# Kernel optimization log

Measured on AMD Instinct MI355X. Metric: run time of the kernel, lower is better.

## Reference

```python
import jax, jax.numpy as jnp
import numpy as np

B, T, C, H = 256, 256, 384, 64
MAX_REL = 3  # max_relative_position hardcoded in module


def setup_inputs() -> dict:
    key = jax.random.key(0)
    ks = jax.random.split(key, 6)
    s = 1.0 / np.sqrt(C)
    return {
        "x": jax.random.normal(ks[0], (B, T, C), dtype=jnp.float32),
        "Wq": jax.random.normal(ks[1], (C, H), dtype=jnp.float32) * s,
        "Wk": jax.random.normal(ks[2], (C, H), dtype=jnp.float32) * s,
        "Wv": jax.random.normal(ks[3], (C, H), dtype=jnp.float32) * s,
        "rel_k_table": jax.random.normal(ks[4], (2 * MAX_REL + 1, H), dtype=jnp.float32) * s,
        "rel_v_table": jax.random.normal(ks[5], (2 * MAX_REL + 1, H), dtype=jnp.float32) * s,
    }


def reference(x, Wq, Wk, Wv, rel_k_table, rel_v_table):
    Bd, Td, Cd = x.shape
    Hd = Wq.shape[1]
    q = x @ Wq  # [B,T,H]
    k = x @ Wk
    v = x @ Wv
    # relative position indices, clipped Shaw-style
    r = jnp.arange(Td)
    idx = jnp.clip(r[None, :] - r[:, None], -MAX_REL, MAX_REL) + MAX_REL  # [T,T]
    rk = rel_k_table[idx]  # [T,T,H]
    rv = rel_v_table[idx]  # [T,T,H]
    attn1 = jnp.einsum('bth,bsh->bts', q, k)
    attn2 = jnp.einsum('bth,tsh->bts', q, rk)
    scale = jnp.sqrt(jnp.asarray(Hd, dtype=x.dtype))
    scores = (attn1 + attn2) / scale
    causal = jnp.tril(jnp.ones((Td, Td), dtype=bool))
    scores = jnp.where(causal[None, :, :], scores, -jnp.inf)
    attn = jax.nn.softmax(scores, axis=-1)  # dropout = identity (eval mode)
    w1 = jnp.einsum('bts,bsh->bth', attn, v)
    w2 = jnp.einsum('bts,tsh->bth', attn, rv)
    return w1 + w2  # [B,T,H]
```

## Files before the change

### kernel.cpp

```cpp
#include <hip/hip_runtime.h>
#include <hip/hip_bf16.h>


typedef __attribute__((ext_vector_type(8))) __bf16 bf16x8;
typedef __attribute__((ext_vector_type(8))) short short8;
typedef __attribute__((ext_vector_type(4))) float f32x4;
typedef __attribute__((ext_vector_type(4))) int   i32x4;

#define MFMA16(A, B, C) __builtin_amdgcn_mfma_f32_16x16x32_bf16((A), (B), (C), 0, 0, 0)

__device__ __forceinline__ unsigned short f2bf(float f) {
    unsigned int u = __builtin_bit_cast(unsigned int, f);
    u = (u + 0x7FFFu + ((u >> 16) & 1u)) >> 16;
    return (unsigned short)u;
}
__device__ __forceinline__ float bf2f(unsigned short s) {
    unsigned int u = ((unsigned int)s) << 16;
    return __builtin_bit_cast(float, u);
}
__device__ __forceinline__ bf16x8 ld16(const unsigned short* p) {
    return __builtin_bit_cast(bf16x8, *(const i32x4*)p);
}

__global__ void prep_wt(const float* __restrict__ Wq, const float* __restrict__ Wk,
                        const float* __restrict__ Wv, const float* __restrict__ relk,
                        unsigned short* __restrict__ Wt, unsigned short* __restrict__ Rk) {
    int i = blockIdx.x * 256 + threadIdx.x;
    if (i < 3 * 64 * 384) {
        int kk = i % 384;
        int h  = (i / 384) & 63;
        int w  = i / (384 * 64);
        const float* W = (w == 0) ? Wq : ((w == 1) ? Wk : Wv);
        Wt[i] = f2bf(W[kk * 64 + h]);
    } else if (i < 3 * 64 * 384 + 1024) {
        int j = i - 3 * 64 * 384;
        int n = j >> 6, h = j & 63;
        Rk[j] = (n < 4) ? f2bf(relk[n * 64 + h]) : (unsigned short)0;
    }
}

__global__ __launch_bounds__(1024)
__attribute__((amdgpu_waves_per_eu(4, 4)))
void fused_kernel(
        const float* __restrict__ x, const unsigned short* __restrict__ Wt,
        const unsigned short* __restrict__ Rk, const float* __restrict__ relv,
        float* __restrict__ out) {
    extern __shared__ unsigned short sh[];
    unsigned short* ws  = sh;
    unsigned short* ksh = sh;
    unsigned short* vTs = sh + 18432;
    unsigned short* qs  = sh + 35328;
    float* lsum = (float*)(sh + 69120);

    const int tid  = threadIdx.x;
    const int wave = tid >> 6;
    const int lane = tid & 63;
    const int c    = lane & 15;
    const int quad = lane >> 4;
    const int b    = blockIdx.x;

    const f32x4 zero = {0.f, 0.f, 0.f, 0.f};

    const float* xcol = x + (size_t)(b * 256 + wave * 16 + c) * 384 + quad * 8;

    f32x4 aq[4], ak[4], av[4];
#pragma unroll
    for (int nt = 0; nt < 4; nt++) { aq[nt] = zero; ak[nt] = zero; av[nt] = zero; }

    f32x4 t[3][2];
#pragma unroll
    for (int j = 0; j < 2; j++) {
        t[j][0] = *(const f32x4*)(xcol + j * 32);
        t[j][1] = *(const f32x4*)(xcol + j * 32 + 4);
    }

#pragma unroll
    for (int it = 0; it < 9; it++) {
        int P_ = it * 1024 + tid;
        int r = P_ / 48, pc = P_ % 48;
        i32x4 d = *(const i32x4*)(Wt + r * 384 + pc * 8);
        *(i32x4*)(ws + r * 392 + pc * 8) = d;
    }
    __syncthreads();

#pragma unroll
    for (int j = 0; j < 12; j++) {
        if (j < 10) {
            t[(j + 2) % 3][0] = *(const f32x4*)(xcol + (j + 2) * 32);
            t[(j + 2) % 3][1] = *(const f32x4*)(xcol + (j + 2) * 32 + 4);
        }
        short8 xs8;
#pragma unroll
        for (int e = 0; e < 4; e++) {
            xs8[e]     = (short)f2bf(t[j % 3][0][e]);
            xs8[4 + e] = (short)f2bf(t[j % 3][1][e]);
        }
        const bf16x8 a = __builtin_bit_cast(bf16x8, xs8);
        const int col = j * 32 + quad * 8;

#pragma unroll
        for (int nt = 0; nt < 4; nt++) {
            bf16x8 bq = ld16(ws + (nt * 16 + c) * 392 + col);
            bf16x8 bk = ld16(ws + (64 + nt * 16 + c) * 392 + col);
            bf16x8 aw = ld16(ws + (128 + nt * 16 + c) * 392 + col);
            aq[nt] = MFMA16(a, bq, aq[nt]);
            ak[nt] = MFMA16(a, bk, ak[nt]);
            av[nt] = MFMA16(aw, a, av[nt]);
        }
    }
    __syncthreads();

#pragma unroll
    for (int nt = 0; nt < 4; nt++)
#pragma unroll
        for (int r = 0; r < 4; r++) {
            int row = wave * 16 + quad * 4 + r;
            qs[row * 72 + nt * 16 + c]  = f2bf(aq[nt][r]);
            ksh[row * 72 + nt * 16 + c] = f2bf(ak[nt][r]);
            vTs[(nt * 16 + quad * 4 + r) * 264 + wave * 16 + c] = f2bf(av[nt][r]);
        }
    __syncthreads();

    const int p  = wave & 7;
    const int hi = wave >> 3;
    const int tA = p, tB = 15 - p;

    bf16x8 qA0 = ld16(qs + (tA * 16 + c) * 72 + quad * 8);
    bf16x8 qA1 = ld16(qs + (tA * 16 + c) * 72 + 32 + quad * 8);
    bf16x8 qB0 = ld16(qs + (tB * 16 + c) * 72 + quad * 8);
    bf16x8 qB1 = ld16(qs + (tB * 16 + c) * 72 + 32 + quad * 8);
    float rv[4][2];
#pragma unroll
    for (int j = 0; j < 4; j++)
#pragma unroll
        for (int i = 0; i < 2; i++)
            rv[j][i] = relv[j * 64 + (hi * 2 + i) * 16 + c];
    __syncthreads();

    unsigned short* Pw = sh + 35328 + p * 4224;

#pragma unroll
    for (int it2 = 0; it2 < 2; it2++) {
        const int tt  = it2 ? tB : tA;
        const bf16x8 aq0 = it2 ? qB0 : qA0;
        const bf16x8 aq1 = it2 ? qB1 : qA1;
        const int nst = tt + 1;

        f32x4 e = zero;
        e = MFMA16(aq0, ld16(Rk + c * 64 + quad * 8), e);
        e = MFMA16(aq1, ld16(Rk + c * 64 + 32 + quad * 8), e);
        float ef[4][4];
#pragma unroll
        for (int r = 0; r < 4; r++)
#pragma unroll
            for (int n = 0; n < 4; n++)
                ef[r][n] = __shfl(e[r], (lane & 48) + n, 64);

        float l[4] = {0.f, 0.f, 0.f, 0.f};
#pragma unroll
        for (int st = 0; st < 16; st++) {
            if ((st & 1) == hi) {
                if (st < nst) {
                    const unsigned short* kp = ksh + (st * 16 + c) * 72 + quad * 8;
                    f32x4 s = zero;
                    s = MFMA16(aq0, ld16(kp), s);
                    s = MFMA16(aq1, ld16(kp + 32), s);
#pragma unroll
                    for (int r = 0; r < 4; r++) {
                        int tg = tt * 16 + quad * 4 + r;
                        int sg = st * 16 + c;
                        int d  = sg - tg;
                        float ee = (d <= -3) ? ef[r][0] : (d == -2) ? ef[r][1]
                                 : (d == -1) ? ef[r][2] : ef[r][3];
                        float pv = (d > 0) ? 0.f : __expf(0.125f * (s[r] + ee));
                        l[r] += pv;
                        Pw[(quad * 4 + r) * 264 + sg] = f2bf(pv);
                    }
                } else if (st == nst && (nst & 1)) {
#pragma unroll
                    for (int r = 0; r < 4; r++)
                        Pw[(quad * 4 + r) * 264 + st * 16 + c] = 0;
                }
            }
        }
#pragma unroll
        for (int r = 0; r < 4; r++)
#pragma unroll
            for (int ofs = 1; ofs < 16; ofs <<= 1)
                l[r] += __shfl_xor(l[r], ofs, 64);
        if (c == 0) {
#pragma unroll
            for (int r = 0; r < 4; r++)
                lsum[(p * 2 + hi) * 16 + quad * 4 + r] = l[r];
        }
        __syncthreads();
        float rl[4];
#pragma unroll
        for (int r = 0; r < 4; r++)
            rl[r] = 1.0f / (l[r] + lsum[(p * 2 + (1 - hi)) * 16 + quad * 4 + r]);

        f32x4 o0[2], o1[2];
        o0[0] = zero; o0[1] = zero; o1[0] = zero; o1[1] = zero;
        const int ksteps = (nst + 1) >> 1;
#pragma unroll
        for (int ks = 0; ks < 8; ks++) {
            if (ks < ksteps) {
                bf16x8 ap = ld16(Pw + c * 264 + ks * 32 + quad * 8);
#pragma unroll
                for (int i = 0; i < 2; i++) {
                    const int nt = hi * 2 + i;
                    bf16x8 bv = ld16(vTs + (nt * 16 + c) * 264 + ks * 32 + quad * 8);
                    if (ks & 1) o1[i] = MFMA16(ap, bv, o1[i]);
                    else        o0[i] = MFMA16(ap, bv, o0[i]);
                }
            }
        }

#pragma unroll
        for (int r = 0; r < 4; r++) {
            int tl = quad * 4 + r;
            int tg = tt * 16 + tl;
            float pa  = (tg >= 2) ? bf2f(Pw[tl * 264 + tg - 2]) * rl[r] : 0.f;
            float pb  = (tg >= 1) ? bf2f(Pw[tl * 264 + tg - 1]) * rl[r] : 0.f;
            float pcv = bf2f(Pw[tl * 264 + tg]) * rl[r];
#pragma unroll
            for (int i = 0; i < 2; i++) {
                const int nt = hi * 2 + i;
                float r0 = rv[0][i];
                float w2 = r0 + pa * (rv[1][i] - r0) + pb * (rv[2][i] - r0)
                              + pcv * (rv[3][i] - r0);
                out[(size_t)(b * 256 + tg) * 64 + nt * 16 + c]
                    = (o0[i][r] + o1[i][r]) * rl[r] + w2;
            }
        }
        __syncthreads();
    }
}

extern "C" void kernel_launch(void* const* d_in, const int* in_sizes, int n_in,
                              void* d_out, int out_size, void* d_ws, size_t ws_size,
                              hipStream_t stream) {
    const float* x    = (const float*)d_in[0];
    const float* Wq   = (const float*)d_in[1];
    const float* Wk   = (const float*)d_in[2];
    const float* Wv   = (const float*)d_in[3];
    const float* relk = (const float*)d_in[4];
    const float* relv = (const float*)d_in[5];
    float* out = (float*)d_out;

    char* ws = (char*)d_ws;
    unsigned short* Wt = (unsigned short*)(ws);
    unsigned short* Rk = (unsigned short*)(ws + 147456);

    (void)hipFuncSetAttribute((const void*)fused_kernel,
                              hipFuncAttributeMaxDynamicSharedMemorySize, 150528);

    prep_wt<<<292, 256, 0, stream>>>(Wq, Wk, Wv, relk, Wt, Rk);
    fused_kernel<<<256, 1024, 150528, stream>>>(x, Wt, Rk, relv, out);
}
```

Before: 195.8 us.

## Halve block to 512 threads, give each wave full row tiles and drop cross-wave softmax sync

The fused kernel now runs 8 waves instead of 16. Each wave projects 32 rows (two row tiles) and reuses the shared weight fragments across both. In attention, each wave handles every key tile and all four head tiles for its query tile pair, so the lsum exchange through shared memory and the per-iteration block barriers are gone. This cuts synchronisation and redundant LDS weight reads, at the cost of fewer waves to hide latency and roughly twice the serial work per wave, with explicit lgkmcnt waits added.

```diff
diff --git a/kernel.cpp b/kernel.cpp
--- a/kernel.cpp
+++ b/kernel.cpp
@@ -39,8 +39,8 @@
     }
 }
 
-__global__ __launch_bounds__(1024)
-__attribute__((amdgpu_waves_per_eu(4, 4)))
+__global__ __launch_bounds__(512)
+__attribute__((amdgpu_waves_per_eu(2, 2)))
 void fused_kernel(
         const float* __restrict__ x, const unsigned short* __restrict__ Wt,
         const unsigned short* __restrict__ Rk, const float* __restrict__ relv,
@@ -50,7 +50,6 @@
     unsigned short* ksh = sh;
     unsigned short* vTs = sh + 18432;
     unsigned short* qs  = sh + 35328;
-    float* lsum = (float*)(sh + 69120);
 
     const int tid  = threadIdx.x;
     const int wave = tid >> 6;
@@ -61,22 +60,27 @@
 
     const f32x4 zero = {0.f, 0.f, 0.f, 0.f};
 
-    const float* xcol = x + (size_t)(b * 256 + wave * 16 + c) * 384 + quad * 8;
-
-    f32x4 aq[4], ak[4], av[4];
-#pragma unroll
-    for (int nt = 0; nt < 4; nt++) { aq[nt] = zero; ak[nt] = zero; av[nt] = zero; }
-
-    f32x4 t[3][2];
+    const float* xc0 = x + (size_t)(b * 256 + wave * 32 + c) * 384 + quad * 8;
+    const float* xc1 = xc0 + 16 * 384;
+
+    f32x4 aq[2][4], ak[2][4], av[2][4];
+#pragma unroll
+    for (int rt = 0; rt < 2; rt++)
+#pragma unroll
+        for (int nt = 0; nt < 4; nt++) { aq[rt][nt] = zero; ak[rt][nt] = zero; av[rt][nt] = zero; }
+
+    f32x4 t[3][2][2];
 #pragma unroll
     for (int j = 0; j < 2; j++) {
-        t[j][0] = *(const f32x4*)(xcol + j * 32);
-        t[j][1] = *(const f32x4*)(xcol + j * 32 + 4);
-    }
-
-#pragma unroll
-    for (int it = 0; it < 9; it++) {
-        int P_ = it * 1024 + tid;
+        t[j][0][0] = *(const f32x4*)(xc0 + j * 32);
+        t[j][0][1] = *(const f32x4*)(xc0 + j * 32 + 4);
+        t[j][1][0] = *(const f32x4*)(xc1 + j * 32);
+        t[j][1][1] = *(const f32x4*)(xc1 + j * 32 + 4);
+    }
+
+#pragma unroll
+    for (int it = 0; it < 18; it++) {
+        int P_ = it * 512 + tid;
         int r = P_ / 48, pc = P_ % 48;
         i32x4 d = *(const i32x4*)(Wt + r * 384 + pc * 8);
         *(i32x4*)(ws + r * 392 + pc * 8) = d;
@@ -86,16 +90,22 @@
 #pragma unroll
     for (int j = 0; j < 12; j++) {
         if (j < 10) {
-            t[(j + 2) % 3][0] = *(const f32x4*)(xcol + (j + 2) * 32);
-            t[(j + 2) % 3][1] = *(const f32x4*)(xcol + (j + 2) * 32 + 4);
-        }
-        short8 xs8;
-#pragma unroll
-        for (int e = 0; e < 4; e++) {
-            xs8[e]     = (short)f2bf(t[j % 3][0][e]);
-            xs8[4 + e] = (short)f2bf(t[j % 3][1][e]);
-        }
-        const bf16x8 a = __builtin_bit_cast(bf16x8, xs8);
+            t[(j + 2) % 3][0][0] = *(const f32x4*)(xc0 + (j + 2) * 32);
+            t[(j + 2) % 3][0][1] = *(const f32x4*)(xc0 + (j + 2) * 32 + 4);
+            t[(j + 2) % 3][1][0] = *(const f32x4*)(xc1 + (j + 2) * 32);
+            t[(j + 2) % 3][1][1] = *(const f32x4*)(xc1 + (j + 2) * 32 + 4);
+        }
+        bf16x8 a[2];
+#pragma unroll
+        for (int rt = 0; rt < 2; rt++) {
+            short8 xs8;
+#pragma unroll
+            for (int e = 0; e < 4; e++) {
+                xs8[e]     = (short)f2bf(t[j % 3][rt][0][e]);
+                xs8[4 + e] = (short)f2bf(t[j % 3][rt][1][e]);
+            }
+            a[rt] = __builtin_bit_cast(bf16x8, xs8);
+        }
         const int col = j * 32 + quad * 8;
 
 #pragma unroll
@@ -103,41 +113,45 @@
             bf16x8 bq = ld16(ws + (nt * 16 + c) * 392 + col);
             bf16x8 bk = ld16(ws + (64 + nt * 16 + c) * 392 + col);
             bf16x8 aw = ld16(ws + (128 + nt * 16 + c) * 392 + col);
-            aq[nt] = MFMA16(a, bq, aq[nt]);
-            ak[nt] = MFMA16(a, bk, ak[nt]);
-            av[nt] = MFMA16(aw, a, av[nt]);
-        }
-    }
-    __syncthreads();
-
-#pragma unroll
-    for (int nt = 0; nt < 4; nt++)
-#pragma unroll
-        for (int r = 0; r < 4; r++) {
-            int row = wave * 16 + quad * 4 + r;
-            qs[row * 72 + nt * 16 + c]  = f2bf(aq[nt][r]);
-            ksh[row * 72 + nt * 16 + c] = f2bf(ak[nt][r]);
-            vTs[(nt * 16 + quad * 4 + r) * 264 + wave * 16 + c] = f2bf(av[nt][r]);
-        }
-    __syncthreads();
-
-    const int p  = wave & 7;
-    const int hi = wave >> 3;
-    const int tA = p, tB = 15 - p;
+            aq[0][nt] = MFMA16(a[0], bq, aq[0][nt]);
+            aq[1][nt] = MFMA16(a[1], bq, aq[1][nt]);
+            ak[0][nt] = MFMA16(a[0], bk, ak[0][nt]);
+            ak[1][nt] = MFMA16(a[1], bk, ak[1][nt]);
+            av[0][nt] = MFMA16(aw, a[0], av[0][nt]);
+            av[1][nt] = MFMA16(aw, a[1], av[1][nt]);
+        }
+    }
+    __syncthreads();
+
+#pragma unroll
+    for (int rt = 0; rt < 2; rt++)
+#pragma unroll
+        for (int nt = 0; nt < 4; nt++)
+#pragma unroll
+            for (int r = 0; r < 4; r++) {
+                int row = wave * 32 + rt * 16 + quad * 4 + r;
+                qs[row * 72 + nt * 16 + c]  = f2bf(aq[rt][nt][r]);
+                ksh[row * 72 + nt * 16 + c] = f2bf(ak[rt][nt][r]);
+                vTs[(nt * 16 + quad * 4 + r) * 264 + wave * 32 + rt * 16 + c]
+                    = f2bf(av[rt][nt][r]);
+            }
+    __syncthreads();
+
+    const int tA = wave, tB = 15 - wave;
 
     bf16x8 qA0 = ld16(qs + (tA * 16 + c) * 72 + quad * 8);
     bf16x8 qA1 = ld16(qs + (tA * 16 + c) * 72 + 32 + quad * 8);
     bf16x8 qB0 = ld16(qs + (tB * 16 + c) * 72 + quad * 8);
     bf16x8 qB1 = ld16(qs + (tB * 16 + c) * 72 + 32 + quad * 8);
-    float rv[4][2];
+    float rv[4][4];
 #pragma unroll
     for (int j = 0; j < 4; j++)
 #pragma unroll
-        for (int i = 0; i < 2; i++)
-            rv[j][i] = relv[j * 64 + (hi * 2 + i) * 16 + c];
-    __syncthreads();
-
-    unsigned short* Pw = sh + 35328 + p * 4224;
+        for (int nt = 0; nt < 4; nt++)
+            rv[j][nt] = relv[j * 64 + nt * 16 + c];
+    __syncthreads();
+
+    unsigned short* Pw = sh + 35328 + wave * 4224;
 
 #pragma unroll
     for (int it2 = 0; it2 < 2; it2++) {
@@ -146,6 +160,8 @@
         const bf16x8 aq1 = it2 ? qB1 : qA1;
         const int nst = tt + 1;
 
+        __asm__ __volatile__("s_waitcnt lgkmcnt(0)" ::: "memory");
+
         f32x4 e = zero;
         e = MFMA16(aq0, ld16(Rk + c * 64 + quad * 8), e);
         e = MFMA16(aq1, ld16(Rk + c * 64 + 32 + quad * 8), e);
@@ -159,28 +175,26 @@
         float l[4] = {0.f, 0.f, 0.f, 0.f};
 #pragma unroll
         for (int st = 0; st < 16; st++) {
-            if ((st & 1) == hi) {
-                if (st < nst) {
-                    const unsigned short* kp = ksh + (st * 16 + c) * 72 + quad * 8;
-                    f32x4 s = zero;
-                    s = MFMA16(aq0, ld16(kp), s);
-                    s = MFMA16(aq1, ld16(kp + 32), s);
-#pragma unroll
-                    for (int r = 0; r < 4; r++) {
-                        int tg = tt * 16 + quad * 4 + r;
-                        int sg = st * 16 + c;
-                        int d  = sg - tg;
-                        float ee = (d <= -3) ? ef[r][0] : (d == -2) ? ef[r][1]
-                                 : (d == -1) ? ef[r][2] : ef[r][3];
-                        float pv = (d > 0) ? 0.f : __expf(0.125f * (s[r] + ee));
-                        l[r] += pv;
-                        Pw[(quad * 4 + r) * 264 + sg] = f2bf(pv);
-                    }
-                } else if (st == nst && (nst & 1)) {
-#pragma unroll
-                    for (int r = 0; r < 4; r++)
-                        Pw[(quad * 4 + r) * 264 + st * 16 + c] = 0;
+            if (st < nst) {
+                const unsigned short* kp = ksh + (st * 16 + c) * 72 + quad * 8;
+                f32x4 s = zero;
+                s = MFMA16(aq0, ld16(kp), s);
+                s = MFMA16(aq1, ld16(kp + 32), s);
+#pragma unroll
+                for (int r = 0; r < 4; r++) {
+                    int tg = tt * 16 + quad * 4 + r;
+                    int sg = st * 16 + c;
+                    int d  = sg - tg;
+                    float ee = (d <= -3) ? ef[r][0] : (d == -2) ? ef[r][1]
+                             : (d == -1) ? ef[r][2] : ef[r][3];
+                    float pv = (d > 0) ? 0.f : __expf(0.125f * (s[r] + ee));
+                    l[r] += pv;
+                    Pw[(quad * 4 + r) * 264 + sg] = f2bf(pv);
                 }
+            } else if (st == nst && (nst & 1)) {
+#pragma unroll
+                for (int r = 0; r < 4; r++)
+                    Pw[(quad * 4 + r) * 264 + st * 16 + c] = 0;
             }
         }
 #pragma unroll
@@ -188,30 +202,25 @@
 #pragma unroll
             for (int ofs = 1; ofs < 16; ofs <<= 1)
                 l[r] += __shfl_xor(l[r], ofs, 64);
-        if (c == 0) {
-#pragma unroll
-            for (int r = 0; r < 4; r++)
-                lsum[(p * 2 + hi) * 16 + quad * 4 + r] = l[r];
-        }
-        __syncthreads();
         float rl[4];
 #pragma unroll
-        for (int r = 0; r < 4; r++)
-            rl[r] = 1.0f / (l[r] + lsum[(p * 2 + (1 - hi)) * 16 + quad * 4 + r]);
-
-        f32x4 o0[2], o1[2];
-        o0[0] = zero; o0[1] = zero; o1[0] = zero; o1[1] = zero;
+        for (int r = 0; r < 4; r++) rl[r] = 1.0f / l[r];
+
+        __asm__ __volatile__("s_waitcnt lgkmcnt(0)" ::: "memory");
+
+        f32x4 o0[4], o1[4];
+#pragma unroll
+        for (int nt = 0; nt < 4; nt++) { o0[nt] = zero; o1[nt] = zero; }
         const int ksteps = (nst + 1) >> 1;
 #pragma unroll
         for (int ks = 0; ks < 8; ks++) {
             if (ks < ksteps) {
                 bf16x8 ap = ld16(Pw + c * 264 + ks * 32 + quad * 8);
 #pragma unroll
-                for (int i = 0; i < 2; i++) {
-                    const int nt = hi * 2 + i;
+                for (int nt = 0; nt < 4; nt++) {
                     bf16x8 bv = ld16(vTs + (nt * 16 + c) * 264 + ks * 32 + quad * 8);
-                    if (ks & 1) o1[i] = MFMA16(ap, bv, o1[i]);
-                    else        o0[i] = MFMA16(ap, bv, o0[i]);
+                    if (ks & 1) o1[nt] = MFMA16(ap, bv, o1[nt]);
+                    else        o0[nt] = MFMA16(ap, bv, o0[nt]);
                 }
             }
         }
@@ -224,16 +233,14 @@
             float pb  = (tg >= 1) ? bf2f(Pw[tl * 264 + tg - 1]) * rl[r] : 0.f;
             float pcv = bf2f(Pw[tl * 264 + tg]) * rl[r];
 #pragma unroll
-            for (int i = 0; i < 2; i++) {
-                const int nt = hi * 2 + i;
-                float r0 = rv[0][i];
-                float w2 = r0 + pa * (rv[1][i] - r0) + pb * (rv[2][i] - r0)
-                              + pcv * (rv[3][i] - r0);
+            for (int nt = 0; nt < 4; nt++) {
+                float r0 = rv[0][nt];
+                float w2 = r0 + pa * (rv[1][nt] - r0) + pb * (rv[2][nt] - r0)
+                              + pcv * (rv[3][nt] - r0);
                 out[(size_t)(b * 256 + tg) * 64 + nt * 16 + c]
-                    = (o0[i][r] + o1[i][r]) * rl[r] + w2;
-            }
-        }
-        __syncthreads();
+                    = (o0[nt][r] + o1[nt][r]) * rl[r] + w2;
+            }
+        }
     }
 }
 
@@ -256,5 +263,5 @@
                               hipFuncAttributeMaxDynamicSharedMemorySize, 150528);
 
     prep_wt<<<292, 256, 0, stream>>>(Wq, Wk, Wv, relk, Wt, Rk);
-    fused_kernel<<<256, 1024, 150528, stream>>>(x, Wt, Rk, relv, out);
-}
+    fused_kernel<<<256, 512, 150528, stream>>>(x, Wt, Rk, relv, out);
+}
```

Result: no change. 197.4 us (+0.8%).
